# Kernel optimization log

Hardware: AMD Instinct MI355X
Metric: run time of the kernel (lower is better)

The kernel has to match this reference:

```python
import jax, jax.numpy as jnp
import numpy as np

D = 256
B, N1, N2 = 4, 512, 512


def setup_inputs() -> dict:
    key = jax.random.key(0)
    k = jax.random.split(key, 6)
    s1 = 1.0 / np.sqrt(2 * D)  # torch Linear init bound ~ U(-1/sqrt(fan_in), ...)
    s2 = 1.0 / np.sqrt(D)
    return {
        "x": jax.random.normal(k[0], (B, N1, D), jnp.float32),
        "y": jax.random.normal(k[1], (B, N2, D), jnp.float32),
        "W1": jax.random.uniform(k[2], (2 * D, D), jnp.float32, -s1, s1),  # linear1.weight.T
        "b1": jax.random.uniform(k[3], (D,), jnp.float32, -s1, s1),
        "W2": jax.random.uniform(k[4], (D, 1), jnp.float32, -s2, s2),  # out.weight.T
        "b2": jax.random.uniform(k[5], (1,), jnp.float32, -s2, s2),
    }


def reference(x, y, W1, b1, W2, b2):
    # linear1 over concat([x,y]) is separable: split W1 into x-part and y-part,
    # project each sequence once, then broadcast-sum over the (n1, n2) grid.
    Wx, Wy = W1[:D], W1[D:]                     # [d, d] each
    xp = jnp.einsum('bnd,de->bne', x, Wx)       # [b, n1, d]
    yp = jnp.einsum('bmd,de->bme', y, Wy)       # [b, n2, d]
    h = xp[:, :, None, :] + yp[:, None, :, :] + b1  # [b, n1, n2, d]
    h = jax.nn.gelu(h, approximate=False)       # torch nn.GELU() is exact erf
    o = jnp.einsum('bnmd,de->bnme', h, W2) + b2  # [b, n1, n2, 1]
    return o[..., 0]                             # [b, n1, n2]
```

## Files before the change

### kernel.cpp

```cpp
#include <hip/hip_runtime.h>

#define DD 256
#define N1 512
#define N2 512
#define BB 4

typedef float f2 __attribute__((ext_vector_type(2)));

__global__ __launch_bounds__(256) void proj_kernel(
    const float* __restrict__ x, const float* __restrict__ y,
    const float* __restrict__ W1, const float* __restrict__ b1,
    float* __restrict__ xp, float* __restrict__ yp)
{
    const int which = blockIdx.z;
    const float* __restrict__ A  = which ? y : x;
    const float* __restrict__ Bw = W1 + which * DD * DD;
    float* __restrict__ outp = which ? yp : xp;

    __shared__ float As[32 * 36];
    __shared__ float Bs[32 * 68];

    const int tid = threadIdx.x;
    const int tx = tid & 15, ty = tid >> 4;
    const int mBase = blockIdx.x * 32;
    const int nBase = blockIdx.y * 64;

    const float4* A4 = (const float4*)A;
    const float4* B4 = (const float4*)Bw;

    const int ar = tid >> 3;
    const int ac = tid & 7;
    const int br = tid >> 4;
    const int bc = tid & 15;

    float4 pa, pb0, pb1;
    pa  = A4[(mBase + ar) * 64 + 0 * 8 + ac];
    pb0 = B4[(0 * 32 + br) * 64 + (nBase >> 2) + bc];
    pb1 = B4[(0 * 32 + br + 16) * 64 + (nBase >> 2) + bc];

    f2 accl[2] = {}, acch[2] = {};

    for (int kc = 0; kc < 8; ++kc) {
        __syncthreads();
        {
            float av[4] = {pa.x, pa.y, pa.z, pa.w};
            #pragma unroll
            for (int q = 0; q < 4; ++q) As[(ac * 4 + q) * 36 + ar] = av[q];
            *(float4*)&Bs[br * 68 + bc * 4] = pb0;
            *(float4*)&Bs[(br + 16) * 68 + bc * 4] = pb1;
        }
        __syncthreads();
        if (kc < 7) {
            pa  = A4[(mBase + ar) * 64 + (kc + 1) * 8 + ac];
            pb0 = B4[((kc + 1) * 32 + br) * 64 + (nBase >> 2) + bc];
            pb1 = B4[((kc + 1) * 32 + br + 16) * 64 + (nBase >> 2) + bc];
        }
        #pragma unroll
        for (int k = 0; k < 32; ++k) {
            f2 a = *(const f2*)&As[k * 36 + ty * 2];
            float4 b = *(const float4*)&Bs[k * 68 + tx * 4];
            f2 blo = {b.x, b.y};
            f2 bhi = {b.z, b.w};
            f2 a0 = {a.x, a.x};
            f2 a1 = {a.y, a.y};
            accl[0] = __builtin_elementwise_fma(a0, blo, accl[0]);
            acch[0] = __builtin_elementwise_fma(a0, bhi, acch[0]);
            accl[1] = __builtin_elementwise_fma(a1, blo, accl[1]);
            acch[1] = __builtin_elementwise_fma(a1, bhi, acch[1]);
        }
    }

    float4 bias = make_float4(0.f, 0.f, 0.f, 0.f);
    if (which == 0) bias = *((const float4*)b1 + (nBase >> 2) + tx);
    #pragma unroll
    for (int i = 0; i < 2; ++i) {
        float4 o;
        o.x = accl[i].x + bias.x;
        o.y = accl[i].y + bias.y;
        o.z = acch[i].x + bias.z;
        o.w = acch[i].y + bias.w;
        ((float4*)outp)[(mBase + ty * 2 + i) * (DD / 4) + (nBase >> 2) + tx] = o;
    }
}

#define GC1  0.79687960f
#define GC3  (-0.13053245f)
#define GC5  0.018104800f
#define GC7  (-0.0017319756f)
#define GC9  1.05671e-4f
#define GC11 (-3.64829e-6f)
#define GC13 5.37117e-8f

__global__ __launch_bounds__(256, 4) void cross_kernel(
    const float* __restrict__ xp, const float* __restrict__ yp,
    const float* __restrict__ W2, const float* __restrict__ b2,
    float* __restrict__ o)
{
    __shared__ float xs[32 * 132];
    __shared__ float ys[16 * 132];

    const int tid   = threadIdx.x;
    const int b     = blockIdx.z;
    const int mBase = blockIdx.x * 16;
    const int nBase = blockIdx.y * 32;
    const int tx = tid & 15;
    const int ty = tid >> 4;

    const float4* xp4 = (const float4*)xp + (b * N1 + nBase) * (DD / 4);
    const float4* yp4 = (const float4*)yp + (b * N2 + mBase) * (DD / 4);
    const float4* __restrict__ W2v = (const float4*)W2;

    const int xsr = tid >> 3;
    const int xsc = tid & 7;
    const int ysr = tid >> 4;
    const int ysc = tid & 15;

    float4 px[4], py[2];
    #pragma unroll
    for (int j = 0; j < 4; ++j) px[j] = xp4[xsr * 64 + xsc + 8 * j];
    #pragma unroll
    for (int j = 0; j < 2; ++j) py[j] = yp4[ysr * 64 + ysc + 16 * j];

    f2 accA[2] = {};
    f2 accB[2] = {};

    for (int kc = 0; kc < 2; ++kc) {
        __syncthreads();
        #pragma unroll
        for (int j = 0; j < 4; ++j)
            *(float4*)&xs[xsr * 132 + (xsc + 8 * j) * 4] = px[j];
        #pragma unroll
        for (int j = 0; j < 2; ++j)
            *(float4*)&ys[ysr * 132 + (ysc + 16 * j) * 4] = py[j];
        __syncthreads();
        if (kc < 1) {
            #pragma unroll
            for (int j = 0; j < 4; ++j) px[j] = xp4[xsr * 64 + 32 + xsc + 8 * j];
            #pragma unroll
            for (int j = 0; j < 2; ++j) py[j] = yp4[ysr * 64 + 32 + ysc + 16 * j];
        }

        #pragma unroll
        for (int c4 = 0; c4 < 32; ++c4) {
            float4 wv = W2v[kc * 32 + c4];
            f2 wlo = {wv.x, wv.y};
            f2 whi = {wv.z, wv.w};
            float4 yr = *(const float4*)&ys[tx * 132 + c4 * 4];
            f2 ylo = {yr.x, yr.y};
            f2 yhi = {yr.z, yr.w};
            #pragma unroll
            for (int i = 0; i < 2; ++i) {
                float4 xr = *(const float4*)&xs[(ty + 16 * i) * 132 + c4 * 4];
                f2 xlo = {xr.x, xr.y};
                f2 xhi = {xr.z, xr.w};
                f2 hlo = xlo + ylo;
                f2 hhi = xhi + yhi;
                f2 ulo = hlo * hlo;
                f2 uhi = hhi * hhi;
                f2 qlo = __builtin_elementwise_fma(ulo, (f2)GC13, (f2)GC11);
                f2 qhi = __builtin_elementwise_fma(uhi, (f2)GC13, (f2)GC11);
                qlo = __builtin_elementwise_fma(qlo, ulo, (f2)GC9);
                qhi = __builtin_elementwise_fma(qhi, uhi, (f2)GC9);
                qlo = __builtin_elementwise_fma(qlo, ulo, (f2)GC7);
                qhi = __builtin_elementwise_fma(qhi, uhi, (f2)GC7);
                qlo = __builtin_elementwise_fma(qlo, ulo, (f2)GC5);
                qhi = __builtin_elementwise_fma(qhi, uhi, (f2)GC5);
                qlo = __builtin_elementwise_fma(qlo, ulo, (f2)GC3);
                qhi = __builtin_elementwise_fma(qhi, uhi, (f2)GC3);
                qlo = __builtin_elementwise_fma(qlo, ulo, (f2)GC1);
                qhi = __builtin_elementwise_fma(qhi, uhi, (f2)GC1);
                f2 slo = __builtin_elementwise_fma(ulo, qlo, hlo);
                f2 shi = __builtin_elementwise_fma(uhi, qhi, hhi);
                accA[i] = __builtin_elementwise_fma(slo, wlo, accA[i]);
                accB[i] = __builtin_elementwise_fma(shi, whi, accB[i]);
            }
        }
    }

    const float bias2 = b2[0];
    const size_t base = ((size_t)(b * N1 + nBase)) * N2 + mBase;
    #pragma unroll
    for (int i = 0; i < 2; ++i) {
        o[base + (size_t)(ty + 16 * i) * N2 + tx] =
            0.5f * (accA[i].x + accA[i].y + accB[i].x + accB[i].y) + bias2;
    }
}

extern "C" void kernel_launch(void* const* d_in, const int* in_sizes, int n_in,
                              void* d_out, int out_size, void* d_ws, size_t ws_size,
                              hipStream_t stream)
{
    const float* x  = (const float*)d_in[0];
    const float* y  = (const float*)d_in[1];
    const float* W1 = (const float*)d_in[2];
    const float* b1 = (const float*)d_in[3];
    const float* W2 = (const float*)d_in[4];
    const float* b2 = (const float*)d_in[5];
    float* o  = (float*)d_out;
    float* xp = (float*)d_ws;
    float* yp = xp + (BB * N1) * DD;

    dim3 g1(64, 4, 2);
    proj_kernel<<<g1, 256, 0, stream>>>(x, y, W1, b1, xp, yp);

    dim3 g2(N2 / 16, N1 / 32, BB);
    cross_kernel<<<g2, 256, 0, stream>>>(xp, yp, W2, b2, o);
}
```

Baseline: 134.4 us.

## Drop LDS staging in cross kernel; read projections directly from global with larger tiles

Measured after the change: 166.1 us. +23.6%, slower.

```diff
diff --git a/kernel.cpp b/kernel.cpp
--- a/kernel.cpp
+++ b/kernel.cpp
@@ -91,89 +91,63 @@
 #define GC11 (-3.64829e-6f)
 #define GC13 5.37117e-8f
 
-__global__ __launch_bounds__(256, 4) void cross_kernel(
+__global__ __launch_bounds__(512, 4) void cross_kernel(
     const float* __restrict__ xp, const float* __restrict__ yp,
     const float* __restrict__ W2, const float* __restrict__ b2,
     float* __restrict__ o)
 {
-    __shared__ float xs[32 * 132];
-    __shared__ float ys[16 * 132];
-
     const int tid   = threadIdx.x;
     const int b     = blockIdx.z;
-    const int mBase = blockIdx.x * 16;
+    const int mBase = blockIdx.x * 32;
     const int nBase = blockIdx.y * 32;
-    const int tx = tid & 15;
-    const int ty = tid >> 4;
+    const int tx = tid & 31;
+    const int ty = tid >> 5;
 
-    const float4* xp4 = (const float4*)xp + (b * N1 + nBase) * (DD / 4);
-    const float4* yp4 = (const float4*)yp + (b * N2 + mBase) * (DD / 4);
+    const float4* __restrict__ xr0p =
+        (const float4*)xp + (size_t)(b * N1 + nBase + ty) * (DD / 4);
+    const float4* __restrict__ xr1p = xr0p + 16 * (DD / 4);
+    const float4* __restrict__ yrp  =
+        (const float4*)yp + (size_t)(b * N2 + mBase + tx) * (DD / 4);
     const float4* __restrict__ W2v = (const float4*)W2;
-
-    const int xsr = tid >> 3;
-    const int xsc = tid & 7;
-    const int ysr = tid >> 4;
-    const int ysc = tid & 15;
-
-    float4 px[4], py[2];
-    #pragma unroll
-    for (int j = 0; j < 4; ++j) px[j] = xp4[xsr * 64 + xsc + 8 * j];
-    #pragma unroll
-    for (int j = 0; j < 2; ++j) py[j] = yp4[ysr * 64 + ysc + 16 * j];
 
     f2 accA[2] = {};
     f2 accB[2] = {};
 
-    for (int kc = 0; kc < 2; ++kc) {
-        __syncthreads();
+    #pragma unroll 16
+    for (int c4 = 0; c4 < 64; ++c4) {
+        float4 wv  = W2v[c4];
+        f2 wlo = {wv.x, wv.y};
+        f2 whi = {wv.z, wv.w};
+        float4 yr  = yrp[c4];
+        f2 ylo = {yr.x, yr.y};
+        f2 yhi = {yr.z, yr.w};
+        float4 xr0 = xr0p[c4];
+        float4 xr1 = xr1p[c4];
         #pragma unroll
-        for (int j = 0; j < 4; ++j)
-            *(float4*)&xs[xsr * 132 + (xsc + 8 * j) * 4] = px[j];
-        #pragma unroll
-        for (int j = 0; j < 2; ++j)
-            *(float4*)&ys[ysr * 132 + (ysc + 16 * j) * 4] = py[j];
-        __syncthreads();
-        if (kc < 1) {
-            #pragma unroll
-            for (int j = 0; j < 4; ++j) px[j] = xp4[xsr * 64 + 32 + xsc + 8 * j];
-            #pragma unroll
-            for (int j = 0; j < 2; ++j) py[j] = yp4[ysr * 64 + 32 + ysc + 16 * j];
-        }
-
-        #pragma unroll
-        for (int c4 = 0; c4 < 32; ++c4) {
-            float4 wv = W2v[kc * 32 + c4];
-            f2 wlo = {wv.x, wv.y};
-            f2 whi = {wv.z, wv.w};
-            float4 yr = *(const float4*)&ys[tx * 132 + c4 * 4];
-            f2 ylo = {yr.x, yr.y};
-            f2 yhi = {yr.z, yr.w};
-            #pragma unroll
-            for (int i = 0; i < 2; ++i) {
-                float4 xr = *(const float4*)&xs[(ty + 16 * i) * 132 + c4 * 4];
-                f2 xlo = {xr.x, xr.y};
-                f2 xhi = {xr.z, xr.w};
-                f2 hlo = xlo + ylo;
-                f2 hhi = xhi + yhi;
-                f2 ulo = hlo * hlo;
-                f2 uhi = hhi * hhi;
-                f2 qlo = __builtin_elementwise_fma(ulo, (f2)GC13, (f2)GC11);
-                f2 qhi = __builtin_elementwise_fma(uhi, (f2)GC13, (f2)GC11);
-                qlo = __builtin_elementwise_fma(qlo, ulo, (f2)GC9);
-                qhi = __builtin_elementwise_fma(qhi, uhi, (f2)GC9);
-                qlo = __builtin_elementwise_fma(qlo, ulo, (f2)GC7);
-                qhi = __builtin_elementwise_fma(qhi, uhi, (f2)GC7);
-                qlo = __builtin_elementwise_fma(qlo, ulo, (f2)GC5);
-                qhi = __builtin_elementwise_fma(qhi, uhi, (f2)GC5);
-                qlo = __builtin_elementwise_fma(qlo, ulo, (f2)GC3);
-                qhi = __builtin_elementwise_fma(qhi, uhi, (f2)GC3);
-                qlo = __builtin_elementwise_fma(qlo, ulo, (f2)GC1);
-                qhi = __builtin_elementwise_fma(qhi, uhi, (f2)GC1);
-                f2 slo = __builtin_elementwise_fma(ulo, qlo, hlo);
-                f2 shi = __builtin_elementwise_fma(uhi, qhi, hhi);
-                accA[i] = __builtin_elementwise_fma(slo, wlo, accA[i]);
-                accB[i] = __builtin_elementwise_fma(shi, whi, accB[i]);
-            }
+        for (int i = 0; i < 2; ++i) {
+            float4 xr = i ? xr1 : xr0;
+            f2 xlo = {xr.x, xr.y};
+            f2 xhi = {xr.z, xr.w};
+            f2 hlo = xlo + ylo;
+            f2 hhi = xhi + yhi;
+            f2 ulo = hlo * hlo;
+            f2 uhi = hhi * hhi;
+            f2 qlo = __builtin_elementwise_fma(ulo, (f2)GC13, (f2)GC11);
+            f2 qhi = __builtin_elementwise_fma(uhi, (f2)GC13, (f2)GC11);
+            qlo = __builtin_elementwise_fma(qlo, ulo, (f2)GC9);
+            qhi = __builtin_elementwise_fma(qhi, uhi, (f2)GC9);
+            qlo = __builtin_elementwise_fma(qlo, ulo, (f2)GC7);
+            qhi = __builtin_elementwise_fma(qhi, uhi, (f2)GC7);
+            qlo = __builtin_elementwise_fma(qlo, ulo, (f2)GC5);
+            qhi = __builtin_elementwise_fma(qhi, uhi, (f2)GC5);
+            qlo = __builtin_elementwise_fma(qlo, ulo, (f2)GC3);
+            qhi = __builtin_elementwise_fma(qhi, uhi, (f2)GC3);
+            qlo = __builtin_elementwise_fma(qlo, ulo, (f2)GC1);
+            qhi = __builtin_elementwise_fma(qhi, uhi, (f2)GC1);
+            f2 slo = __builtin_elementwise_fma(ulo, qlo, hlo);
+            f2 shi = __builtin_elementwise_fma(uhi, qhi, hhi);
+            accA[i] = __builtin_elementwise_fma(slo, wlo, accA[i]);
+            accB[i] = __builtin_elementwise_fma(shi, whi, accB[i]);
         }
     }
 
@@ -203,6 +177,6 @@
     dim3 g1(64, 4, 2);
     proj_kernel<<<g1, 256, 0, stream>>>(x, y, W1, b1, xp, yp);
 
-    dim3 g2(N2 / 16, N1 / 32, BB);
-    cross_kernel<<<g2, 256, 0, stream>>>(xp, yp, W2, b2, o);
+    dim3 g2(N2 / 32, N1 / 32, BB);
+    cross_kernel<<<g2, 512, 0, stream>>>(xp, yp, W2, b2, o);
 }
```
